# Performance work log

Hardware: AMD Instinct MI355X
Metric: run time of the kernel (lower is better)

The kernel has to match this reference:

```python
import jax, jax.numpy as jnp
import numpy as np

N_QUBITS = 14
N_LOCAL = 3
VQC_DEPTH = 6
BATCH = 512
NLOC = 2 ** N_LOCAL            # 8 = Hermitian dimension
NOFF = NLOC * (NLOC - 1) // 2  # 28 off-diagonal params
_ROWS, _COLS = np.tril_indices(NLOC, -1)  # row-major order matches the torch nested loop


def _make_hermitian(a, b, d):
    # Faithful to create_Hermitian: h[i,j]=A[k]+iB[k] for j<i (row-major over i=1..N-1),
    # h[i-1,i-1]=D[i] for i=1..N-1 (D[0] unused, last diag 0), then H = h + h^H.
    tri = jnp.zeros((NLOC, NLOC), jnp.complex64).at[_ROWS, _COLS].set(a + 1j * b)
    diag = jnp.concatenate([d[1:], jnp.zeros(1, d.dtype)]).astype(jnp.complex64)
    h = tri + jnp.diag(diag)
    return h + h.conj().T


def _apply_ry(state, angle, wire):
    # state: (B, 2, 2, ..., 2); angle: scalar (shared) or (B,) per-sample
    half = 0.5 * angle
    c, s = jnp.cos(half), jnp.sin(half)
    if jnp.ndim(angle) == 1:
        bshape = (angle.shape[0],) + (1,) * (N_QUBITS - 1)
        c, s = c.reshape(bshape), s.reshape(bshape)
    s0 = jnp.take(state, 0, axis=wire + 1)
    s1 = jnp.take(state, 1, axis=wire + 1)
    return jnp.stack([c * s0 - s * s1, s * s0 + c * s1], axis=wire + 1)


def _apply_cnot(state, ctrl):
    # CNOT with target = ctrl + 1 (the only pattern used by entangling_layer)
    ax = ctrl + 1
    s0 = jnp.take(state, 0, axis=ax)
    s1 = jnp.take(state, 1, axis=ax)
    # after removing the control axis, the target axis sits at position ax
    s1 = jnp.flip(s1, axis=ax)
    return jnp.stack([s0, s1], axis=ax)


def _circuit(X, theta, H):
    B = X.shape[0]
    # Hadamard layer applied to |0...0> yields the uniform superposition
    amp = 1.0 / np.sqrt(2.0 ** N_QUBITS)
    state = jnp.full((B,) + (2,) * N_QUBITS, amp, dtype=jnp.complex64)
    for w in range(N_QUBITS):
        state = _apply_ry(state, X[:, w], w)
    for k in range(VQC_DEPTH):
        for i in range(0, N_QUBITS - 1, 2):
            state = _apply_cnot(state, i)
        for i in range(1, N_QUBITS - 1, 2):
            state = _apply_cnot(state, i)
        for w in range(N_QUBITS):
            state = _apply_ry(state, theta[k, w], w)
    exps = []
    for q in range(N_QUBITS):
        wires = [(q + j) % N_QUBITS for j in range(N_LOCAL)]
        psi = jnp.moveaxis(state, [w + 1 for w in wires], list(range(1, N_LOCAL + 1)))
        psi = psi.reshape(B, NLOC, -1)  # (B, 8, 2^(n-3))
        e = jnp.einsum('bir,ij,bjr->b', psi.conj(), H[q], psi).real
        exps.append(e)
    return jnp.stack(exps, axis=1).astype(jnp.float32)  # (B, n_qubits)


def setup_inputs() -> dict:
    key = jax.random.key(0)
    k = jax.random.split(key, 5)
    X = jax.random.normal(k[0], (BATCH, N_QUBITS), jnp.float32)
    theta = 0.01 * jax.random.normal(k[1], (VQC_DEPTH, N_QUBITS), jnp.float32)
    A = 2.0 * jax.random.normal(k[2], (N_QUBITS, NOFF), jnp.float32)
    Bp = 2.0 * jax.random.normal(k[3], (N_QUBITS, NOFF), jnp.float32)
    D = 2.0 * jax.random.normal(k[4], (N_QUBITS, NLOC), jnp.float32)
    return {"X": X, "theta": theta, "A": A, "B": Bp, "D": D}


def reference(X, theta, A, B, D):
    H = jax.vmap(_make_hermitian)(A, B, D)  # (n_qubits, 8, 8) complex64
    q_out = _circuit(X, theta, H)
    return q_out[:, :2]
```

## Files before the change

### kernel.cpp

```cpp
#include <hip/hip_runtime.h>
#include <math.h>

#define NQ 14
#define NSTATE (1 << 14)
#define DEPTH  6
#define NT     1024

typedef float v2f __attribute__((ext_vector_type(2)));

__device__ __forceinline__ int swz(int n) { return n ^ ((n >> 4) & 28); }

__device__ __forceinline__ int sigma(int n) {
    int m = n ^ ((n & 0x1554) >> 1);
    return m ^ ((m & 0x2AAA) >> 1);
}

__device__ __forceinline__ v2f pkmul_cc(v2f a, v2f cs) {
    v2f d;
    asm("v_pk_mul_f32 %0, %1, %2 op_sel:[0,0] op_sel_hi:[1,0]"
        : "=v"(d) : "v"(a), "v"(cs));
    return d;
}
__device__ __forceinline__ v2f pkmul_ss(v2f a, v2f cs) {
    v2f d;
    asm("v_pk_mul_f32 %0, %1, %2 op_sel:[0,1] op_sel_hi:[1,1]"
        : "=v"(d) : "v"(a), "v"(cs));
    return d;
}
__device__ __forceinline__ v2f pkfma_cc(v2f a, v2f cs, v2f acc) {
    v2f d;
    asm("v_pk_fma_f32 %0, %1, %2, %3 op_sel:[0,0,0] op_sel_hi:[1,0,1]"
        : "=v"(d) : "v"(a), "v"(cs), "v"(acc));
    return d;
}
__device__ __forceinline__ v2f pkfma_nss(v2f a, v2f cs, v2f acc) {
    v2f d;
    asm("v_pk_fma_f32 %0, %1, %2, %3 op_sel:[0,1,0] op_sel_hi:[1,1,1] neg_lo:[0,1,0] neg_hi:[0,1,0]"
        : "=v"(d) : "v"(a), "v"(cs), "v"(acc));
    return d;
}
__device__ __forceinline__ v2f pkfma_sw(v2f a, v2f cs, v2f acc) {
    v2f d;
    asm("v_pk_fma_f32 %0, %1, %2, %3 op_sel:[1,1,0] op_sel_hi:[0,1,1] neg_lo:[0,1,0] neg_hi:[0,0,0]"
        : "=v"(d) : "v"(a), "v"(cs), "v"(acc));
    return d;
}

__device__ __forceinline__ void ry_pk0(float (&p)[16], v2f cs) {
#pragma unroll
    for (int j = 0; j < 8; ++j) {
        v2f v = *(v2f*)&p[2 * j];
        *(v2f*)&p[2 * j] = pkfma_sw(v, cs, pkmul_cc(v, cs));
    }
}
template <int JB>
__device__ __forceinline__ void ry_pkN(float (&p)[16], v2f cs) {
#pragma unroll
    for (int j = 0; j < 8; ++j) {
        if (!((j >> (JB - 1)) & 1)) {
            const int j1 = j | (1 << (JB - 1));
            v2f a0 = *(v2f*)&p[2 * j], a1 = *(v2f*)&p[2 * j1];
            *(v2f*)&p[2 * j]  = pkfma_nss(a1, cs, pkmul_cc(a0, cs));
            *(v2f*)&p[2 * j1] = pkfma_cc(a1, cs, pkmul_ss(a0, cs));
        }
    }
}
__device__ __forceinline__ void ry4_pk(float (&p)[16], float2 q0, float2 q1,
                                       float2 q2, float2 q3) {
    v2f c0, c1, c2, c3;
    c0.x = q0.x; c0.y = q0.y;
    c1.x = q1.x; c1.y = q1.y;
    c2.x = q2.x; c2.y = q2.y;
    c3.x = q3.x; c3.y = q3.y;
    ry_pk0(p, c0);
    ry_pkN<1>(p, c1);
    ry_pkN<2>(p, c2);
    ry_pkN<3>(p, c3);
}

template <int CTRL>
__device__ __forceinline__ void ry_dpp(float (&p)[16], float c, float sg) {
#pragma unroll
    for (int i = 0; i < 16; ++i) {
        float partner = __int_as_float(__builtin_amdgcn_update_dpp(
            0, __float_as_int(p[i]), CTRL, 0xF, 0xF, true));
        p[i] = c * p[i] + sg * partner;
    }
}

__global__ __launch_bounds__(NT, 4)
void vqc_kernel(const float* __restrict__ X,
                const float* __restrict__ TH,
                const float* __restrict__ A,
                const float* __restrict__ Bc,
                const float* __restrict__ D,
                float* __restrict__ out)
{
    __shared__ __align__(16) float st[NSTATE];
    __shared__ float2 tb[DEPTH * NQ];
    __shared__ float2 xf[NQ];
    __shared__ float  red[2 * (NT / 64)];

    const int t = threadIdx.x;
    const int b = blockIdx.x;

    if (t < DEPTH * NQ) {
        float s, c;
        __sincosf(0.5f * TH[t], &s, &c);
        tb[t] = make_float2(c, s);
    } else if (t < DEPTH * NQ + NQ) {
        const int j = t - DEPTH * NQ;
        float s, c;
        __sincosf(0.5f * X[b * NQ + (13 - j)], &s, &c);
        xf[j] = make_float2(c - s, c + s);
    }
    __syncthreads();

    {
        const int mt = sigma(t << 4);
        float sh = 1.0f / 128.0f;
#pragma unroll
        for (int j = 4; j < 14; ++j) {
            float2 f = xf[j];
            sh *= ((mt >> j) & 1) ? f.y : f.x;
        }
        float fa[4], fb[4];
#pragma unroll
        for (int j = 0; j < 4; ++j) {
            float2 f = xf[j];
            const int mj = (mt >> j) & 1;
            fa[j] = mj ? f.y : f.x;
            fb[j] = mj ? f.x : f.y;
        }
        float p[16];
#pragma unroll
        for (int i = 0; i < 16; ++i) {
            const int sl = sigma(i);
            float v = sh;
            v *= (sl & 1)        ? fb[0] : fa[0];
            v *= ((sl >> 1) & 1) ? fb[1] : fa[1];
            v *= ((sl >> 2) & 1) ? fb[2] : fa[2];
            v *= ((sl >> 3) & 1) ? fb[3] : fa[3];
            p[i] = v;
        }
        ry4_pk(p, tb[13], tb[12], tb[11], tb[10]);
        const int wb = swz(t << 4);
#pragma unroll
        for (int g = 0; g < 4; ++g)
            *(float4*)&st[wb ^ (g << 2)] =
                make_float4(p[4 * g], p[4 * g + 1], p[4 * g + 2], p[4 * g + 3]);
    }
    __syncthreads();

    for (int k = 0; k < DEPTH; ++k) {
        const float2* tbk = tb + k * NQ;

        if (k > 0) {
            const int rb = swz(sigma(t << 4) & ~15) ^ ((t & 1) * 12);
            float tmpf[16];
#pragma unroll
            for (int g = 0; g < 4; ++g)
                *(float4*)&tmpf[g * 4] = *(const float4*)&st[rb ^ (g << 2)];
            float p[16];
#pragma unroll
            for (int i = 0; i < 16; ++i) {
                const int i0 = i & 1, i1 = (i >> 1) & 1, i2 = (i >> 2) & 1, i3 = (i >> 3) & 1;
                const int s = (i0 ^ i1 ^ i2) | ((i1 ^ i2) << 1) | ((i2 ^ i3) << 2) | (i3 << 3);
                p[i] = tmpf[s];
            }
            __syncthreads();
            ry4_pk(p, tbk[13], tbk[12], tbk[11], tbk[10]);
            const int wb = swz(t << 4);
#pragma unroll
            for (int g = 0; g < 4; ++g)
                *(float4*)&st[wb ^ (g << 2)] =
                    make_float4(p[4 * g], p[4 * g + 1], p[4 * g + 2], p[4 * g + 3]);
            __syncthreads();
        }

        {
            const int raw = ((t >> 2) & 15) | ((t & 1) << 8) | ((t & 2) << 8)
                          | (((t >> 6) & 15) << 10);
            const int base2 = swz(raw);
            float p[16];
#pragma unroll
            for (int ip = 0; ip < 16; ++ip) {
                if ((ip & 2) == 0) {
                    const int v = base2 ^ (ip << 4) ^ (ip & 12);
                    p[ip]     = st[v];
                    p[ip | 2] = st[v + 32];
                }
            }
            ry4_pk(p, tbk[9], tbk[8], tbk[7], tbk[6]);
            float2 w5 = tbk[5], w4 = tbk[4];
            const float sg5 = (t & 1) ? w5.y : -w5.y;
            const float sg4 = (t & 2) ? w4.y : -w4.y;
            ry_dpp<0xB1>(p, w5.x, sg5);
            ry_dpp<0x4E>(p, w4.x, sg4);
#pragma unroll
            for (int ip = 0; ip < 16; ++ip) {
                if ((ip & 2) == 0) {
                    const int v = base2 ^ (ip << 4) ^ (ip & 12);
                    st[v]      = p[ip];
                    st[v + 32] = p[ip | 2];
                }
            }
            __syncthreads();
        }

        {
            const int base3 = swz(t);
            float p[16];
#pragma unroll
            for (int i = 0; i < 16; ++i) p[i] = st[base3 + (i << 10)];
            ry4_pk(p, tbk[3], tbk[2], tbk[1], tbk[0]);
#pragma unroll
            for (int i = 0; i < 16; ++i) st[base3 + (i << 10)] = p[i];
            __syncthreads();
        }
    }

    float e[2];
#pragma unroll
    for (int q = 0; q < 2; ++q) {
        const int shift = 11 - q;
        float dg[8];
#pragma unroll
        for (int i = 0; i < 7; ++i) dg[i] = 2.0f * D[q * 8 + i + 1];
        dg[7] = 0.0f;
        float acc = 0.0f;
        const int lowmask = (1 << shift) - 1;
        for (int r = t; r < NSTATE / 8; r += NT) {
            const int base = ((r >> shift) << (shift + 3)) | (r & lowmask);
            float ps[8];
#pragma unroll
            for (int i = 0; i < 8; ++i) ps[i] = st[swz(base + (i << shift))];
#pragma unroll
            for (int i = 0; i < 8; ++i) acc += dg[i] * ps[i] * ps[i];
            int kk = 0;
#pragma unroll
            for (int i = 1; i < 8; ++i)
#pragma unroll
                for (int j = 0; j < i; ++j, ++kk)
                    acc += 2.0f * A[q * 28 + kk] * ps[i] * ps[j];
        }
        e[q] = acc;
    }

    float v0 = e[0], v1 = e[1];
#pragma unroll
    for (int o = 32; o > 0; o >>= 1) {
        v0 += __shfl_down(v0, o);
        v1 += __shfl_down(v1, o);
    }
    if ((t & 63) == 0) {
        red[(t >> 6) * 2]     = v0;
        red[(t >> 6) * 2 + 1] = v1;
    }
    __syncthreads();
    if (t == 0) {
        float s0 = 0.0f, s1 = 0.0f;
#pragma unroll
        for (int i = 0; i < NT / 64; ++i) { s0 += red[i * 2]; s1 += red[i * 2 + 1]; }
        out[b * 2 + 0] = s0;
        out[b * 2 + 1] = s1;
    }
}

extern "C" void kernel_launch(void* const* d_in, const int* in_sizes, int n_in,
                              void* d_out, int out_size, void* d_ws, size_t ws_size,
                              hipStream_t stream) {
    const float* X  = (const float*)d_in[0];
    const float* TH = (const float*)d_in[1];
    const float* A  = (const float*)d_in[2];
    const float* Bc = (const float*)d_in[3];
    const float* D  = (const float*)d_in[4];
    float* out = (float*)d_out;
    vqc_kernel<<<512, NT, 0, stream>>>(X, TH, A, Bc, D, out);
}
```

Measured before the change: 45.50 us.

## Process two batch samples per block and pack DPP rotation into pk_fma

Each 1024-thread block now simulates two state vectors (two samples) in a double shared-memory buffer, halving the grid to 256 blocks and the number of barriers per sample. The point is to amortise __syncthreads and the per-gate setup over twice the work and to interleave independent instruction streams. Separately, the DPP-based RY gates are rewritten to use packed v_pk_fma/v_pk_mul on pairs. The cost is doubled LDS (128KB per block) and register pressure, plus fewer blocks than there are CUs, which can reduce occupancy and GPU fill.

After: 49.73 us. 9.3% more time.

```diff
diff --git a/kernel.cpp b/kernel.cpp
--- a/kernel.cpp
+++ b/kernel.cpp
@@ -43,6 +43,12 @@
     v2f d;
     asm("v_pk_fma_f32 %0, %1, %2, %3 op_sel:[1,1,0] op_sel_hi:[0,1,1] neg_lo:[0,1,0] neg_hi:[0,0,0]"
         : "=v"(d) : "v"(a), "v"(cs), "v"(acc));
+    return d;
+}
+__device__ __forceinline__ v2f pkfma(v2f a, v2f bb, v2f acc) {
+    v2f d;
+    asm("v_pk_fma_f32 %0, %1, %2, %3"
+        : "=v"(d) : "v"(a), "v"(bb), "v"(acc));
     return d;
 }
 
@@ -79,13 +85,81 @@
 }
 
 template <int CTRL>
-__device__ __forceinline__ void ry_dpp(float (&p)[16], float c, float sg) {
+__device__ __forceinline__ void ry_dpp_pk(float (&p)[16], float c, float sg) {
+    v2f cs; cs.x = c; cs.y = 0.0f;
+    v2f sgv; sgv.x = sg; sgv.y = sg;
+#pragma unroll
+    for (int j = 0; j < 8; ++j) {
+        v2f pt;
+        pt.x = __int_as_float(__builtin_amdgcn_update_dpp(
+            0, __float_as_int(p[2 * j]), CTRL, 0xF, 0xF, true));
+        pt.y = __int_as_float(__builtin_amdgcn_update_dpp(
+            0, __float_as_int(p[2 * j + 1]), CTRL, 0xF, 0xF, true));
+        v2f v = *(v2f*)&p[2 * j];
+        *(v2f*)&p[2 * j] = pkfma(pt, sgv, pkmul_cc(v, cs));
+    }
+}
+
+__device__ __forceinline__ void init_product(const float2* __restrict__ xfs,
+                                             int mt, float (&p)[16]) {
+    float sh = 1.0f / 128.0f;
+#pragma unroll
+    for (int j = 4; j < 14; ++j) {
+        float2 f = xfs[j];
+        sh *= ((mt >> j) & 1) ? f.y : f.x;
+    }
+    float fa[4], fb[4];
+#pragma unroll
+    for (int j = 0; j < 4; ++j) {
+        float2 f = xfs[j];
+        const int mj = (mt >> j) & 1;
+        fa[j] = mj ? f.y : f.x;
+        fb[j] = mj ? f.x : f.y;
+    }
 #pragma unroll
     for (int i = 0; i < 16; ++i) {
-        float partner = __int_as_float(__builtin_amdgcn_update_dpp(
-            0, __float_as_int(p[i]), CTRL, 0xF, 0xF, true));
-        p[i] = c * p[i] + sg * partner;
-    }
+        const int sl = sigma(i);
+        float v = sh;
+        v *= (sl & 1)        ? fb[0] : fa[0];
+        v *= ((sl >> 1) & 1) ? fb[1] : fa[1];
+        v *= ((sl >> 2) & 1) ? fb[2] : fa[2];
+        v *= ((sl >> 3) & 1) ? fb[3] : fa[3];
+        p[i] = v;
+    }
+}
+
+__device__ __forceinline__ void expect2(const float* __restrict__ stt,
+                                        const float* __restrict__ A,
+                                        const float* __restrict__ D,
+                                        int t, float& E0, float& E1) {
+    float e[2];
+#pragma unroll
+    for (int q = 0; q < 2; ++q) {
+        const int shift = 11 - q;
+        float dg[8];
+#pragma unroll
+        for (int i = 0; i < 7; ++i) dg[i] = 2.0f * D[q * 8 + i + 1];
+        dg[7] = 0.0f;
+        float acc = 0.0f;
+        const int lowmask = (1 << shift) - 1;
+        for (int r = t; r < NSTATE / 8; r += NT) {
+            const int base = ((r >> shift) << (shift + 3)) | (r & lowmask);
+            float ps[8];
+#pragma unroll
+            for (int i = 0; i < 8; ++i) ps[i] = stt[swz(base + (i << shift))];
+#pragma unroll
+            for (int i = 0; i < 8; ++i) acc += dg[i] * ps[i] * ps[i];
+            int kk = 0;
+#pragma unroll
+            for (int i = 1; i < 8; ++i)
+#pragma unroll
+                for (int j = 0; j < i; ++j, ++kk)
+                    acc += 2.0f * A[q * 28 + kk] * ps[i] * ps[j];
+        }
+        e[q] = acc;
+    }
+    E0 = e[0];
+    E1 = e[1];
 }
 
 __global__ __launch_bounds__(NT, 4)
@@ -96,59 +170,44 @@
                 const float* __restrict__ D,
                 float* __restrict__ out)
 {
-    __shared__ __align__(16) float st[NSTATE];
+    __shared__ __align__(16) float st[2][NSTATE];
     __shared__ float2 tb[DEPTH * NQ];
-    __shared__ float2 xf[NQ];
-    __shared__ float  red[2 * (NT / 64)];
-
-    const int t = threadIdx.x;
-    const int b = blockIdx.x;
+    __shared__ float2 xf[2][NQ];
+    __shared__ float  red[4 * (NT / 64)];
+
+    const int t  = threadIdx.x;
+    const int b0 = blockIdx.x * 2;
 
     if (t < DEPTH * NQ) {
         float s, c;
         __sincosf(0.5f * TH[t], &s, &c);
         tb[t] = make_float2(c, s);
-    } else if (t < DEPTH * NQ + NQ) {
-        const int j = t - DEPTH * NQ;
+    } else if (t < DEPTH * NQ + 2 * NQ) {
+        const int j  = t - DEPTH * NQ;
+        const int sm = j < NQ ? 0 : 1;
+        const int jj = j < NQ ? j : j - NQ;
         float s, c;
-        __sincosf(0.5f * X[b * NQ + (13 - j)], &s, &c);
-        xf[j] = make_float2(c - s, c + s);
+        __sincosf(0.5f * X[(b0 + sm) * NQ + (13 - jj)], &s, &c);
+        xf[sm][jj] = make_float2(c - s, c + s);
     }
     __syncthreads();
+
+    float pA[16], pB[16];
 
     {
         const int mt = sigma(t << 4);
-        float sh = 1.0f / 128.0f;
-#pragma unroll
-        for (int j = 4; j < 14; ++j) {
-            float2 f = xf[j];
-            sh *= ((mt >> j) & 1) ? f.y : f.x;
-        }
-        float fa[4], fb[4];
-#pragma unroll
-        for (int j = 0; j < 4; ++j) {
-            float2 f = xf[j];
-            const int mj = (mt >> j) & 1;
-            fa[j] = mj ? f.y : f.x;
-            fb[j] = mj ? f.x : f.y;
-        }
-        float p[16];
-#pragma unroll
-        for (int i = 0; i < 16; ++i) {
-            const int sl = sigma(i);
-            float v = sh;
-            v *= (sl & 1)        ? fb[0] : fa[0];
-            v *= ((sl >> 1) & 1) ? fb[1] : fa[1];
-            v *= ((sl >> 2) & 1) ? fb[2] : fa[2];
-            v *= ((sl >> 3) & 1) ? fb[3] : fa[3];
-            p[i] = v;
-        }
-        ry4_pk(p, tb[13], tb[12], tb[11], tb[10]);
+        init_product(xf[0], mt, pA);
+        init_product(xf[1], mt, pB);
+        ry4_pk(pA, tb[13], tb[12], tb[11], tb[10]);
+        ry4_pk(pB, tb[13], tb[12], tb[11], tb[10]);
         const int wb = swz(t << 4);
 #pragma unroll
-        for (int g = 0; g < 4; ++g)
-            *(float4*)&st[wb ^ (g << 2)] =
-                make_float4(p[4 * g], p[4 * g + 1], p[4 * g + 2], p[4 * g + 3]);
+        for (int g = 0; g < 4; ++g) {
+            *(float4*)&st[0][wb ^ (g << 2)] =
+                make_float4(pA[4 * g], pA[4 * g + 1], pA[4 * g + 2], pA[4 * g + 3]);
+            *(float4*)&st[1][wb ^ (g << 2)] =
+                make_float4(pB[4 * g], pB[4 * g + 1], pB[4 * g + 2], pB[4 * g + 3]);
+        }
     }
     __syncthreads();
 
@@ -157,24 +216,30 @@
 
         if (k > 0) {
             const int rb = swz(sigma(t << 4) & ~15) ^ ((t & 1) * 12);
-            float tmpf[16];
-#pragma unroll
-            for (int g = 0; g < 4; ++g)
-                *(float4*)&tmpf[g * 4] = *(const float4*)&st[rb ^ (g << 2)];
-            float p[16];
+            float tA[16], tB[16];
+#pragma unroll
+            for (int g = 0; g < 4; ++g) {
+                *(float4*)&tA[g * 4] = *(const float4*)&st[0][rb ^ (g << 2)];
+                *(float4*)&tB[g * 4] = *(const float4*)&st[1][rb ^ (g << 2)];
+            }
 #pragma unroll
             for (int i = 0; i < 16; ++i) {
                 const int i0 = i & 1, i1 = (i >> 1) & 1, i2 = (i >> 2) & 1, i3 = (i >> 3) & 1;
                 const int s = (i0 ^ i1 ^ i2) | ((i1 ^ i2) << 1) | ((i2 ^ i3) << 2) | (i3 << 3);
-                p[i] = tmpf[s];
+                pA[i] = tA[s];
+                pB[i] = tB[s];
             }
             __syncthreads();
-            ry4_pk(p, tbk[13], tbk[12], tbk[11], tbk[10]);
+            ry4_pk(pA, tbk[13], tbk[12], tbk[11], tbk[10]);
+            ry4_pk(pB, tbk[13], tbk[12], tbk[11], tbk[10]);
             const int wb = swz(t << 4);
 #pragma unroll
-            for (int g = 0; g < 4; ++g)
-                *(float4*)&st[wb ^ (g << 2)] =
-                    make_float4(p[4 * g], p[4 * g + 1], p[4 * g + 2], p[4 * g + 3]);
+            for (int g = 0; g < 4; ++g) {
+                *(float4*)&st[0][wb ^ (g << 2)] =
+                    make_float4(pA[4 * g], pA[4 * g + 1], pA[4 * g + 2], pA[4 * g + 3]);
+                *(float4*)&st[1][wb ^ (g << 2)] =
+                    make_float4(pB[4 * g], pB[4 * g + 1], pB[4 * g + 2], pB[4 * g + 3]);
+            }
             __syncthreads();
         }
 
@@ -182,27 +247,33 @@
             const int raw = ((t >> 2) & 15) | ((t & 1) << 8) | ((t & 2) << 8)
                           | (((t >> 6) & 15) << 10);
             const int base2 = swz(raw);
-            float p[16];
 #pragma unroll
             for (int ip = 0; ip < 16; ++ip) {
                 if ((ip & 2) == 0) {
                     const int v = base2 ^ (ip << 4) ^ (ip & 12);
-                    p[ip]     = st[v];
-                    p[ip | 2] = st[v + 32];
+                    pA[ip]     = st[0][v];
+                    pA[ip | 2] = st[0][v + 32];
+                    pB[ip]     = st[1][v];
+                    pB[ip | 2] = st[1][v + 32];
                 }
             }
-            ry4_pk(p, tbk[9], tbk[8], tbk[7], tbk[6]);
+            ry4_pk(pA, tbk[9], tbk[8], tbk[7], tbk[6]);
+            ry4_pk(pB, tbk[9], tbk[8], tbk[7], tbk[6]);
             float2 w5 = tbk[5], w4 = tbk[4];
             const float sg5 = (t & 1) ? w5.y : -w5.y;
             const float sg4 = (t & 2) ? w4.y : -w4.y;
-            ry_dpp<0xB1>(p, w5.x, sg5);
-            ry_dpp<0x4E>(p, w4.x, sg4);
+            ry_dpp_pk<0xB1>(pA, w5.x, sg5);
+            ry_dpp_pk<0xB1>(pB, w5.x, sg5);
+            ry_dpp_pk<0x4E>(pA, w4.x, sg4);
+            ry_dpp_pk<0x4E>(pB, w4.x, sg4);
 #pragma unroll
             for (int ip = 0; ip < 16; ++ip) {
                 if ((ip & 2) == 0) {
                     const int v = base2 ^ (ip << 4) ^ (ip & 12);
-                    st[v]      = p[ip];
-                    st[v + 32] = p[ip | 2];
+                    st[0][v]      = pA[ip];
+                    st[0][v + 32] = pA[ip | 2];
+                    st[1][v]      = pB[ip];
+                    st[1][v + 32] = pB[ip | 2];
                 }
             }
             __syncthreads();
@@ -210,60 +281,53 @@
 
         {
             const int base3 = swz(t);
-            float p[16];
-#pragma unroll
-            for (int i = 0; i < 16; ++i) p[i] = st[base3 + (i << 10)];
-            ry4_pk(p, tbk[3], tbk[2], tbk[1], tbk[0]);
-#pragma unroll
-            for (int i = 0; i < 16; ++i) st[base3 + (i << 10)] = p[i];
+#pragma unroll
+            for (int i = 0; i < 16; ++i) {
+                pA[i] = st[0][base3 + (i << 10)];
+                pB[i] = st[1][base3 + (i << 10)];
+            }
+            ry4_pk(pA, tbk[3], tbk[2], tbk[1], tbk[0]);
+            ry4_pk(pB, tbk[3], tbk[2], tbk[1], tbk[0]);
+#pragma unroll
+            for (int i = 0; i < 16; ++i) {
+                st[0][base3 + (i << 10)] = pA[i];
+                st[1][base3 + (i << 10)] = pB[i];
+            }
             __syncthreads();
         }
     }
 
-    float e[2];
-#pragma unroll
-    for (int q = 0; q < 2; ++q) {
-        const int shift = 11 - q;
-        float dg[8];
-#pragma unroll
-        for (int i = 0; i < 7; ++i) dg[i] = 2.0f * D[q * 8 + i + 1];
-        dg[7] = 0.0f;
-        float acc = 0.0f;
-        const int lowmask = (1 << shift) - 1;
-        for (int r = t; r < NSTATE / 8; r += NT) {
-            const int base = ((r >> shift) << (shift + 3)) | (r & lowmask);
-            float ps[8];
-#pragma unroll
-            for (int i = 0; i < 8; ++i) ps[i] = st[swz(base + (i << shift))];
-#pragma unroll
-            for (int i = 0; i < 8; ++i) acc += dg[i] * ps[i] * ps[i];
-            int kk = 0;
-#pragma unroll
-            for (int i = 1; i < 8; ++i)
-#pragma unroll
-                for (int j = 0; j < i; ++j, ++kk)
-                    acc += 2.0f * A[q * 28 + kk] * ps[i] * ps[j];
-        }
-        e[q] = acc;
-    }
-
-    float v0 = e[0], v1 = e[1];
+    float eA0, eA1, eB0, eB1;
+    expect2(st[0], A, D, t, eA0, eA1);
+    expect2(st[1], A, D, t, eB0, eB1);
+
 #pragma unroll
     for (int o = 32; o > 0; o >>= 1) {
-        v0 += __shfl_down(v0, o);
-        v1 += __shfl_down(v1, o);
+        eA0 += __shfl_down(eA0, o);
+        eA1 += __shfl_down(eA1, o);
+        eB0 += __shfl_down(eB0, o);
+        eB1 += __shfl_down(eB1, o);
     }
     if ((t & 63) == 0) {
-        red[(t >> 6) * 2]     = v0;
-        red[(t >> 6) * 2 + 1] = v1;
+        red[(t >> 6) * 4 + 0] = eA0;
+        red[(t >> 6) * 4 + 1] = eA1;
+        red[(t >> 6) * 4 + 2] = eB0;
+        red[(t >> 6) * 4 + 3] = eB1;
     }
     __syncthreads();
     if (t == 0) {
-        float s0 = 0.0f, s1 = 0.0f;
-#pragma unroll
-        for (int i = 0; i < NT / 64; ++i) { s0 += red[i * 2]; s1 += red[i * 2 + 1]; }
-        out[b * 2 + 0] = s0;
-        out[b * 2 + 1] = s1;
+        float s0 = 0.0f, s1 = 0.0f, s2 = 0.0f, s3 = 0.0f;
+#pragma unroll
+        for (int i = 0; i < NT / 64; ++i) {
+            s0 += red[i * 4 + 0];
+            s1 += red[i * 4 + 1];
+            s2 += red[i * 4 + 2];
+            s3 += red[i * 4 + 3];
+        }
+        out[b0 * 2 + 0]       = s0;
+        out[b0 * 2 + 1]       = s1;
+        out[(b0 + 1) * 2 + 0] = s2;
+        out[(b0 + 1) * 2 + 1] = s3;
     }
 }
 
@@ -276,5 +340,5 @@
     const float* Bc = (const float*)d_in[3];
     const float* D  = (const float*)d_in[4];
     float* out = (float*)d_out;
-    vqc_kernel<<<512, NT, 0, stream>>>(X, TH, A, Bc, D, out);
-}
+    vqc_kernel<<<256, NT, 0, stream>>>(X, TH, A, Bc, D, out);
+}
```

## Merge middle and high-qubit stages via DPP cross-lane rotations

Applied to the files above, without the earlier changes.

Moves the RY gates for qubits 8-9 into the first stage using DPP lane swaps. It then merges the old middle stage into the last stage by mapping qubits 4-7 onto lane bits and applying them with DPP, using composed row_mirror/row_half_mirror patterns for the larger lane strides. This removes one full LDS read/write pass and one barrier per depth layer, at the cost of more cross-lane DPP operations. The single-lane DPP update is also rewritten with packed FMA. Correctness of the composed DPP patterns for the 4- and 8-lane strides is the main risk.

Measured after the change: 49.11 us. 7.9% more time.

```diff
diff --git a/kernel.cpp b/kernel.cpp
--- a/kernel.cpp
+++ b/kernel.cpp
@@ -43,6 +43,12 @@
     v2f d;
     asm("v_pk_fma_f32 %0, %1, %2, %3 op_sel:[1,1,0] op_sel_hi:[0,1,1] neg_lo:[0,1,0] neg_hi:[0,0,0]"
         : "=v"(d) : "v"(a), "v"(cs), "v"(acc));
+    return d;
+}
+__device__ __forceinline__ v2f pkfma(v2f a, v2f bb, v2f acc) {
+    v2f d;
+    asm("v_pk_fma_f32 %0, %1, %2, %3"
+        : "=v"(d) : "v"(a), "v"(bb), "v"(acc));
     return d;
 }
 
@@ -79,12 +85,38 @@
 }
 
 template <int CTRL>
-__device__ __forceinline__ void ry_dpp(float (&p)[16], float c, float sg) {
-#pragma unroll
-    for (int i = 0; i < 16; ++i) {
-        float partner = __int_as_float(__builtin_amdgcn_update_dpp(
-            0, __float_as_int(p[i]), CTRL, 0xF, 0xF, true));
-        p[i] = c * p[i] + sg * partner;
+__device__ __forceinline__ void ry_dpp_pk(float (&p)[16], float c, float sg) {
+    v2f cs; cs.x = c; cs.y = 0.0f;
+    v2f sgv; sgv.x = sg; sgv.y = sg;
+#pragma unroll
+    for (int j = 0; j < 8; ++j) {
+        v2f pt;
+        pt.x = __int_as_float(__builtin_amdgcn_update_dpp(
+            0, __float_as_int(p[2 * j]), CTRL, 0xF, 0xF, true));
+        pt.y = __int_as_float(__builtin_amdgcn_update_dpp(
+            0, __float_as_int(p[2 * j + 1]), CTRL, 0xF, 0xF, true));
+        v2f v = *(v2f*)&p[2 * j];
+        *(v2f*)&p[2 * j] = pkfma(pt, sgv, pkmul_cc(v, cs));
+    }
+}
+
+template <int C1, int C2>
+__device__ __forceinline__ void ry_dpp2_pk(float (&p)[16], float c, float sg) {
+    v2f cs; cs.x = c; cs.y = 0.0f;
+    v2f sgv; sgv.x = sg; sgv.y = sg;
+#pragma unroll
+    for (int j = 0; j < 8; ++j) {
+        v2f pt;
+        int ax = __builtin_amdgcn_update_dpp(
+            0, __float_as_int(p[2 * j]), C1, 0xF, 0xF, true);
+        pt.x = __int_as_float(__builtin_amdgcn_update_dpp(
+            0, ax, C2, 0xF, 0xF, true));
+        int ay = __builtin_amdgcn_update_dpp(
+            0, __float_as_int(p[2 * j + 1]), C1, 0xF, 0xF, true);
+        pt.y = __int_as_float(__builtin_amdgcn_update_dpp(
+            0, ay, C2, 0xF, 0xF, true));
+        v2f v = *(v2f*)&p[2 * j];
+        *(v2f*)&p[2 * j] = pkfma(pt, sgv, pkmul_cc(v, cs));
     }
 }
 
@@ -144,6 +176,11 @@
             p[i] = v;
         }
         ry4_pk(p, tb[13], tb[12], tb[11], tb[10]);
+        float2 w9 = tb[9], w8 = tb[8];
+        const float sg9 = (t & 1) ? w9.y : -w9.y;
+        const float sg8 = (t & 2) ? w8.y : -w8.y;
+        ry_dpp_pk<0xB1>(p, w9.x, sg9);
+        ry_dpp_pk<0x4E>(p, w8.x, sg8);
         const int wb = swz(t << 4);
 #pragma unroll
         for (int g = 0; g < 4; ++g)
@@ -170,6 +207,11 @@
             }
             __syncthreads();
             ry4_pk(p, tbk[13], tbk[12], tbk[11], tbk[10]);
+            float2 w9 = tbk[9], w8 = tbk[8];
+            const float sg9 = (t & 1) ? w9.y : -w9.y;
+            const float sg8 = (t & 2) ? w8.y : -w8.y;
+            ry_dpp_pk<0xB1>(p, w9.x, sg9);
+            ry_dpp_pk<0x4E>(p, w8.x, sg8);
             const int wb = swz(t << 4);
 #pragma unroll
             for (int g = 0; g < 4; ++g)
@@ -179,43 +221,24 @@
         }
 
         {
-            const int raw = ((t >> 2) & 15) | ((t & 1) << 8) | ((t & 2) << 8)
-                          | (((t >> 6) & 15) << 10);
+            const int raw = ((t >> 4) & 3) | (((t >> 6) & 15) << 2)
+                          | ((t & 3) << 6) | (((t >> 2) & 3) << 8);
             const int base2 = swz(raw);
             float p[16];
 #pragma unroll
-            for (int ip = 0; ip < 16; ++ip) {
-                if ((ip & 2) == 0) {
-                    const int v = base2 ^ (ip << 4) ^ (ip & 12);
-                    p[ip]     = st[v];
-                    p[ip | 2] = st[v + 32];
-                }
-            }
-            ry4_pk(p, tbk[9], tbk[8], tbk[7], tbk[6]);
-            float2 w5 = tbk[5], w4 = tbk[4];
-            const float sg5 = (t & 1) ? w5.y : -w5.y;
-            const float sg4 = (t & 2) ? w4.y : -w4.y;
-            ry_dpp<0xB1>(p, w5.x, sg5);
-            ry_dpp<0x4E>(p, w4.x, sg4);
-#pragma unroll
-            for (int ip = 0; ip < 16; ++ip) {
-                if ((ip & 2) == 0) {
-                    const int v = base2 ^ (ip << 4) ^ (ip & 12);
-                    st[v]      = p[ip];
-                    st[v + 32] = p[ip | 2];
-                }
-            }
-            __syncthreads();
-        }
-
-        {
-            const int base3 = swz(t);
-            float p[16];
-#pragma unroll
-            for (int i = 0; i < 16; ++i) p[i] = st[base3 + (i << 10)];
+            for (int i = 0; i < 16; ++i) p[i] = st[base2 + (i << 10)];
             ry4_pk(p, tbk[3], tbk[2], tbk[1], tbk[0]);
-#pragma unroll
-            for (int i = 0; i < 16; ++i) st[base3 + (i << 10)] = p[i];
+            float2 w7 = tbk[7], w6 = tbk[6], w5 = tbk[5], w4 = tbk[4];
+            const float sg7 = (t & 1) ? w7.y : -w7.y;
+            const float sg6 = (t & 2) ? w6.y : -w6.y;
+            const float sg5 = (t & 4) ? w5.y : -w5.y;
+            const float sg4 = (t & 8) ? w4.y : -w4.y;
+            ry_dpp_pk<0xB1>(p, w7.x, sg7);
+            ry_dpp_pk<0x4E>(p, w6.x, sg6);
+            ry_dpp2_pk<0x1B, 0x141>(p, w5.x, sg5);
+            ry_dpp2_pk<0x141, 0x140>(p, w4.x, sg4);
+#pragma unroll
+            for (int i = 0; i < 16; ++i) st[base2 + (i << 10)] = p[i];
             __syncthreads();
         }
     }
```
